# Optimization experiments

Measured on AMD Instinct MI355X. Metric: run time of the kernel, lower is better.

## Reference

```python
import jax, jax.numpy as jnp
import numpy as np

D = 64          # embed_dim
NH = 4          # nhead
DH = D // NH    # head dim
FF = 2048       # TransformerEncoderLayer default dim_feedforward
V = 1_000_000   # vocab (num items)
MAX_LEN = 50
INSERT_LEN = 10
EPS = 1e-5
N_LAYERS = 2


def setup_inputs() -> dict:
    key = jax.random.key(0)
    ks = jax.random.split(key, 8)
    s = 0.02
    return {
        "ht": jax.random.normal(ks[0], (D,), dtype=jnp.float32),
        "item_emb": jax.random.normal(ks[1], (V, D), dtype=jnp.float32) * s,
        "pos_emb": jax.random.normal(ks[2], (MAX_LEN, D), dtype=jnp.float32) * s,
        "in_proj_w": jax.random.normal(ks[3], (N_LAYERS, 3 * D, D), dtype=jnp.float32) * s,
        "in_proj_b": jnp.zeros((N_LAYERS, 3 * D), jnp.float32),
        "out_w": jax.random.normal(ks[4], (N_LAYERS, D, D), dtype=jnp.float32) * s,
        "out_b": jnp.zeros((N_LAYERS, D), jnp.float32),
        "ln1_w": jnp.ones((N_LAYERS, D), jnp.float32),
        "ln1_b": jnp.zeros((N_LAYERS, D), jnp.float32),
        "ln2_w": jnp.ones((N_LAYERS, D), jnp.float32),
        "ln2_b": jnp.zeros((N_LAYERS, D), jnp.float32),
        "ffn1_w": jax.random.normal(ks[5], (N_LAYERS, FF, D), dtype=jnp.float32) * s,
        "ffn1_b": jnp.zeros((N_LAYERS, FF), jnp.float32),
        "ffn2_w": jax.random.normal(ks[6], (N_LAYERS, D, FF), dtype=jnp.float32) * s,
        "ffn2_b": jnp.zeros((N_LAYERS, D), jnp.float32),
    }


def _ln(x, w, b):
    m = jnp.mean(x, axis=-1, keepdims=True)
    v = jnp.mean(jnp.square(x - m), axis=-1, keepdims=True)
    return (x - m) * jax.lax.rsqrt(v + EPS) * w + b


def _encoder_layer(x, ipw, ipb, ow, ob, l1w, l1b, l2w, l2b, f1w, f1b, f2w, f2b):
    # x: [S, D]; post-norm TransformerEncoderLayer (PyTorch defaults, eval mode)
    S = x.shape[0]
    qkv = x @ ipw.T + ipb                      # [S, 3D]
    q, k, v = jnp.split(qkv, 3, axis=-1)
    q = q.reshape(S, NH, DH)
    k = k.reshape(S, NH, DH)
    v = v.reshape(S, NH, DH)
    scores = jnp.einsum('shd,thd->hst', q, k) / jnp.sqrt(jnp.float32(DH))
    attn = jax.nn.softmax(scores, axis=-1)
    o = jnp.einsum('hst,thd->shd', attn, v).reshape(S, D)
    o = o @ ow.T + ob
    x = _ln(x + o, l1w, l1b)
    ff = jax.nn.relu(x @ f1w.T + f1b) @ f2w.T + f2b
    return _ln(x + ff, l2w, l2b)


def reference(ht, item_emb, pos_emb, in_proj_w, in_proj_b, out_w, out_b,
              ln1_w, ln1_b, ln2_w, ln2_b, ffn1_w, ffn1_b, ffn2_w, ffn2_b):
    gen = []         # generated item indices (traced int scalars)
    logits_all = []
    for _ in range(INSERT_LEN):
        if gen:
            gen_embed = item_emb[jnp.stack(gen)]             # [t, D]
            stack = jnp.concatenate([ht[None, :], gen_embed], axis=0)
        else:
            stack = ht[None, :]
        S = stack.shape[0]
        x = stack + pos_emb[:S]
        for l in range(N_LAYERS):
            x = _encoder_layer(x, in_proj_w[l], in_proj_b[l], out_w[l], out_b[l],
                               ln1_w[l], ln1_b[l], ln2_w[l], ln2_b[l],
                               ffn1_w[l], ffn1_b[l], ffn2_w[l], ffn2_b[l])
        logits = x[-1] @ item_emb.T                           # [V]
        gen.append(jnp.argmax(logits))
        logits_all.append(logits)
    return jnp.stack(logits_all), jnp.stack(gen)
```

## Files before the change

### kernel.cpp

```cpp
#include <hip/hip_runtime.h>

typedef unsigned long long u64;
typedef unsigned int u32;
typedef unsigned short u16;

#define V_ 1000000
#define STEPS_ 10
#define EPS_ 1e-5f
#define MARGIN_ 0.02f

__device__ __forceinline__ u64 pack_best(float v, int idx) {
    u32 u = __float_as_uint(v);
    u = (u & 0x80000000u) ? ~u : (u | 0x80000000u);
    return ((u64)u << 32) | (u64)(~(u32)idx);
}
__device__ __forceinline__ int unpack_idx(u64 p) { return (int)(~(u32)p); }
__device__ __forceinline__ float unpack_val(u64 p) {
    u32 hi = (u32)(p >> 32);
    return __uint_as_float((hi & 0x80000000u) ? (hi ^ 0x80000000u) : ~hi);
}
__device__ __forceinline__ u64 shfl_xor_u64(u64 v, int m) {
    u32 lo = (u32)v, hi = (u32)(v >> 32);
    lo = (u32)__shfl_xor((int)lo, m);
    hi = (u32)__shfl_xor((int)hi, m);
    return ((u64)hi << 32) | lo;
}
__device__ __forceinline__ u16 f2bf(float f) {
    u32 u = __float_as_uint(f);
    u += 0x7fffu + ((u >> 16) & 1u);
    return (u16)(u >> 16);
}
__device__ __forceinline__ float bf_lo(u32 u) { return __uint_as_float(u << 16); }
__device__ __forceinline__ float bf_hi(u32 u) { return __uint_as_float(u & 0xffff0000u); }

__device__ int resolve_argmax(const u64* __restrict__ cand,
                              const float* __restrict__ item_emb,
                              const float* __restrict__ y_last,
                              const float* __restrict__ lnw,
                              const float* __restrict__ lnb,
                              float* s_xl, int* s_list, u64* s_wm,
                              int* s_cnt, u64* s_best)
{
    const int tid = threadIdx.x;
    if (tid < 64) {
        float v = y_last[tid];
        float m = v;
        #pragma unroll
        for (int o = 1; o < 64; o <<= 1) m += __shfl_xor(m, o);
        m *= (1.f / 64.f);
        float df = v - m;
        float var = df * df;
        #pragma unroll
        for (int o = 1; o < 64; o <<= 1) var += __shfl_xor(var, o);
        var *= (1.f / 64.f);
        s_xl[tid] = df * (1.f / sqrtf(var + EPS_)) * lnw[tid] + lnb[tid];
    }
    if (tid == 0) { *s_cnt = 0; *s_best = 0ull; }
    __syncthreads();

    u64 m = 0ull;
    for (int i = tid; i < 2048; i += 256) { u64 c = cand[i]; if (c > m) m = c; }
    #pragma unroll
    for (int o = 1; o < 64; o <<= 1) { u64 x = shfl_xor_u64(m, o); if (x > m) m = x; }
    if ((tid & 63) == 0) s_wm[tid >> 6] = m;
    __syncthreads();
    if (tid == 0) {
        u64 b = s_wm[0];
        for (int i = 1; i < 4; i++) if (s_wm[i] > b) b = s_wm[i];
        s_wm[0] = b;
    }
    __syncthreads();

    float thr = unpack_val(s_wm[0]) - MARGIN_;
    for (int i = tid; i < 2048; i += 256) {
        if (unpack_val(cand[i]) >= thr) {
            int p = atomicAdd(s_cnt, 1);
            if (p < 64) s_list[p] = unpack_idx(cand[i]);
        }
    }
    __syncthreads();
    int n = *s_cnt; if (n > 64) n = 64;
    const int wid = tid >> 6, lane = tid & 63;
    for (int c = wid; c < n; c += 4) {
        int row = s_list[c];
        float p = s_xl[lane] * item_emb[(size_t)row * 64 + lane];
        #pragma unroll
        for (int o = 1; o < 64; o <<= 1) p += __shfl_xor(p, o);
        if (lane == 0) atomicMax(s_best, pack_best(p, row));
    }
    __syncthreads();
    return unpack_idx(*s_best);
}

__global__ __launch_bounds__(256) void attn0_kernel(
    const float* __restrict__ ht, const float* __restrict__ item_emb,
    const float* __restrict__ pos_emb,
    const float* __restrict__ ipw, const float* __restrict__ ipb,
    const float* __restrict__ ow,  const float* __restrict__ ob,
    const float* __restrict__ l1w, const float* __restrict__ l1b,
    const float* __restrict__ l2w1, const float* __restrict__ l2b1,
    const u64* __restrict__ cand, const float* __restrict__ y_last,
    int* __restrict__ gen_idx, float* __restrict__ gen_out,
    const float* __restrict__ f1w, const float* __restrict__ f1b,
    float* __restrict__ xp0, float* __restrict__ hbuf, int t)
{
    const int S = t + 1;
    const int tid = threadIdx.x;
    __shared__ float x[640], qkv[1920], att[400], o_[640], y2[640], xps[640];
    __shared__ float rm[10], rr[10], xl[64];
    __shared__ int list[64], cnt;
    __shared__ u64 wm[4], best;

    int newidx = -1;
    if (t > 0) {
        newidx = resolve_argmax(cand, item_emb, y_last, l2w1, l2b1,
                                xl, list, wm, &cnt, &best);
        if (blockIdx.x == 0 && tid == 0) {
            gen_idx[t - 1] = newidx;
            gen_out[t - 1] = (float)newidx;
        }
    }
    __syncthreads();

    for (int i = tid; i < S * 64; i += 256) {
        int s = i >> 6, d = i & 63;
        float base;
        if (s == 0) base = ht[d];
        else {
            int gi = (s == t) ? newidx : gen_idx[s - 1];
            base = item_emb[(size_t)gi * 64 + d];
        }
        x[i] = base + pos_emb[i];
    }
    __syncthreads();

    for (int i = tid; i < S * 192; i += 256) {
        int s = i / 192, j = i % 192;
        float acc = ipb[j];
        const float4* wr = (const float4*)(ipw + j * 64);
        const float4* xr = (const float4*)(x + s * 64);
        #pragma unroll
        for (int k = 0; k < 16; k++) {
            float4 w4 = wr[k], xv = xr[k];
            acc += w4.x * xv.x + w4.y * xv.y + w4.z * xv.z + w4.w * xv.w;
        }
        qkv[i] = acc;
    }
    __syncthreads();

    for (int i = tid; i < 4 * S * S; i += 256) {
        int h = i / (S * S), r = i % (S * S);
        int si = r / S, ti = r % S;
        const float* qr = qkv + si * 192 + h * 16;
        const float* kr = qkv + ti * 192 + 64 + h * 16;
        float acc = 0.f;
        #pragma unroll
        for (int k = 0; k < 16; k++) acc += qr[k] * kr[k];
        att[(h * S + si) * S + ti] = acc * 0.25f;
    }
    __syncthreads();

    for (int i = tid; i < 4 * S; i += 256) {
        float* row = att + i * S;
        float mx = row[0];
        for (int j = 1; j < S; j++) mx = fmaxf(mx, row[j]);
        float sm = 0.f;
        for (int j = 0; j < S; j++) { float e = expf(row[j] - mx); row[j] = e; sm += e; }
        float inv = 1.f / sm;
        for (int j = 0; j < S; j++) row[j] *= inv;
    }
    __syncthreads();

    for (int i = tid; i < S * 64; i += 256) {
        int si = i >> 6, d = i & 63, h = d >> 4, dh = d & 15;
        const float* ar = att + (h * S + si) * S;
        float acc = 0.f;
        for (int ti = 0; ti < S; ti++) acc += ar[ti] * qkv[ti * 192 + 128 + h * 16 + dh];
        o_[i] = acc;
    }
    __syncthreads();

    for (int i = tid; i < S * 64; i += 256) {
        int s = i >> 6, d = i & 63;
        float acc = ob[d] + x[i];
        const float4* wr = (const float4*)(ow + d * 64);
        const float4* orow = (const float4*)(o_ + s * 64);
        #pragma unroll
        for (int k = 0; k < 16; k++) {
            float4 w4 = wr[k], ov = orow[k];
            acc += w4.x * ov.x + w4.y * ov.y + w4.z * ov.z + w4.w * ov.w;
        }
        y2[i] = acc;
    }
    __syncthreads();

    if (tid < S) {
        const float* yr = y2 + tid * 64;
        float m = 0.f;
        for (int k = 0; k < 64; k++) m += yr[k];
        m *= (1.f / 64.f);
        float v = 0.f;
        for (int k = 0; k < 64; k++) { float df = yr[k] - m; v += df * df; }
        rm[tid] = m;
        rr[tid] = 1.f / sqrtf(v * (1.f / 64.f) + EPS_);
    }
    __syncthreads();
    for (int i = tid; i < S * 64; i += 256) {
        int s = i >> 6, d = i & 63;
        float v = (y2[i] - rm[s]) * rr[s] * l1w[d] + l1b[d];
        xps[i] = v;
        xp0[i] = v;
    }
    __syncthreads();

    const int jl = tid >> 4, kp = tid & 15;
    const int j = blockIdx.x * 16 + jl;
    float4 w4 = ((const float4*)(f1w + (size_t)j * 64))[kp];
    float b1 = f1b[j];
    for (int s = 0; s < S; s++) {
        float4 xv = ((const float4*)(xps + s * 64))[kp];
        float p = w4.x * xv.x + w4.y * xv.y + w4.z * xv.z + w4.w * xv.w;
        p += __shfl_xor(p, 1);
        p += __shfl_xor(p, 2);
        p += __shfl_xor(p, 4);
        p += __shfl_xor(p, 8);
        if (kp == 0) hbuf[s * 2048 + j] = fmaxf(p + b1, 0.f);
    }
}

__global__ __launch_bounds__(256) void ffn2_full_kernel(
    const float* __restrict__ f2w0, const float* __restrict__ f2b0,
    const float* __restrict__ hbuf, const float* __restrict__ xp0,
    float* __restrict__ y0, int S)
{
    const int tid = threadIdx.x, d = blockIdx.x;
    const float4* w4 = (const float4*)(f2w0 + (size_t)d * 2048 + tid * 8);
    float4 w0 = w4[0], w1 = w4[1];
    __shared__ float sw[4][10];
    for (int s = 0; s < S; s++) {
        const float4* h4 = (const float4*)(hbuf + s * 2048 + tid * 8);
        float4 h0 = h4[0], h1 = h4[1];
        float p = w0.x * h0.x + w0.y * h0.y + w0.z * h0.z + w0.w * h0.w
                + w1.x * h1.x + w1.y * h1.y + w1.z * h1.z + w1.w * h1.w;
        #pragma unroll
        for (int o = 1; o < 64; o <<= 1) p += __shfl_xor(p, o);
        if ((tid & 63) == 0) sw[tid >> 6][s] = p;
    }
    __syncthreads();
    if (tid < S)
        y0[tid * 64 + d] = sw[0][tid] + sw[1][tid] + sw[2][tid] + sw[3][tid]
                         + f2b0[d] + xp0[tid * 64 + d];
}

__global__ __launch_bounds__(256) void attn1_kernel(
    const float* __restrict__ y0,
    const float* __restrict__ l2w0, const float* __restrict__ l2b0,
    const float* __restrict__ ipw1, const float* __restrict__ ipb1,
    const float* __restrict__ ow1,  const float* __restrict__ ob1,
    const float* __restrict__ l1w1, const float* __restrict__ l1b1,
    const float* __restrict__ f1w1, const float* __restrict__ f1b1,
    float* __restrict__ xp1_last, float* __restrict__ hbuf, int S)
{
    const int tid = threadIdx.x;
    __shared__ float y0s[640], x1[640], qkv[1920], att[40], ol[64], y2l[64], xpl[64];
    __shared__ float rm[10], rr[10];

    for (int i = tid; i < S * 64; i += 256) y0s[i] = y0[i];
    __syncthreads();
    if (tid < S) {
        const float* yr = y0s + tid * 64;
        float m = 0.f;
        for (int k = 0; k < 64; k++) m += yr[k];
        m *= (1.f / 64.f);
        float v = 0.f;
        for (int k = 0; k < 64; k++) { float df = yr[k] - m; v += df * df; }
        rm[tid] = m;
        rr[tid] = 1.f / sqrtf(v * (1.f / 64.f) + EPS_);
    }
    __syncthreads();
    for (int i = tid; i < S * 64; i += 256) {
        int s = i >> 6, d = i & 63;
        x1[i] = (y0s[i] - rm[s]) * rr[s] * l2w0[d] + l2b0[d];
    }
    __syncthreads();

    for (int i = tid; i < S * 192; i += 256) {
        int s = i / 192, j = i % 192;
        float acc = ipb1[j];
        const float4* wr = (const float4*)(ipw1 + j * 64);
        const float4* xr = (const float4*)(x1 + s * 64);
        #pragma unroll
        for (int k = 0; k < 16; k++) {
            float4 w4 = wr[k], xv = xr[k];
            acc += w4.x * xv.x + w4.y * xv.y + w4.z * xv.z + w4.w * xv.w;
        }
        qkv[i] = acc;
    }
    __syncthreads();

    for (int i = tid; i < 4 * S; i += 256) {
        int h = i / S, ti = i % S;
        const float* qr = qkv + (S - 1) * 192 + h * 16;
        const float* kr = qkv + ti * 192 + 64 + h * 16;
        float acc = 0.f;
        #pragma unroll
        for (int k = 0; k < 16; k++) acc += qr[k] * kr[k];
        att[h * S + ti] = acc * 0.25f;
    }
    __syncthreads();
    if (tid < 4) {
        float* row = att + tid * S;
        float mx = row[0];
        for (int j = 1; j < S; j++) mx = fmaxf(mx, row[j]);
        float sm = 0.f;
        for (int j = 0; j < S; j++) { float e = expf(row[j] - mx); row[j] = e; sm += e; }
        float inv = 1.f / sm;
        for (int j = 0; j < S; j++) row[j] *= inv;
    }
    __syncthreads();
    if (tid < 64) {
        int h = tid >> 4, dh = tid & 15;
        const float* ar = att + h * S;
        float acc = 0.f;
        for (int ti = 0; ti < S; ti++) acc += ar[ti] * qkv[ti * 192 + 128 + h * 16 + dh];
        ol[tid] = acc;
    }
    __syncthreads();
    if (tid < 64) {
        float acc = ob1[tid] + x1[(S - 1) * 64 + tid];
        const float* wr = ow1 + tid * 64;
        for (int k = 0; k < 64; k++) acc += ol[k] * wr[k];
        y2l[tid] = acc;
    }
    __syncthreads();
    if (tid < 64) {
        float v = y2l[tid];
        float m = v;
        #pragma unroll
        for (int o = 1; o < 64; o <<= 1) m += __shfl_xor(m, o);
        m *= (1.f / 64.f);
        float df = v - m;
        float var = df * df;
        #pragma unroll
        for (int o = 1; o < 64; o <<= 1) var += __shfl_xor(var, o);
        float r = 1.f / sqrtf(var * (1.f / 64.f) + EPS_);
        float xv = df * r * l1w1[tid] + l1b1[tid];
        xpl[tid] = xv;
        xp1_last[tid] = xv;
    }
    __syncthreads();

    const int jl = tid >> 4, kp = tid & 15;
    const int j = blockIdx.x * 16 + jl;
    float4 w4 = ((const float4*)(f1w1 + (size_t)j * 64))[kp];
    float4 xv = ((const float4*)xpl)[kp];
    float p = w4.x * xv.x + w4.y * xv.y + w4.z * xv.z + w4.w * xv.w;
    p += __shfl_xor(p, 1);
    p += __shfl_xor(p, 2);
    p += __shfl_xor(p, 4);
    p += __shfl_xor(p, 8);
    if (kp == 0) hbuf[j] = fmaxf(p + f1b1[j], 0.f);
}

__global__ __launch_bounds__(256) void ffn2_last_kernel(
    const float* __restrict__ f2w1, const float* __restrict__ f2b1,
    const float* __restrict__ hbuf, const float* __restrict__ xp1_last,
    float* __restrict__ y_last)
{
    const int tid = threadIdx.x, d = blockIdx.x;
    const float4* w4 = (const float4*)(f2w1 + (size_t)d * 2048 + tid * 8);
    const float4* h4 = (const float4*)(hbuf + tid * 8);
    float4 w0 = w4[0], w1 = w4[1], h0 = h4[0], h1 = h4[1];
    float p = w0.x * h0.x + w0.y * h0.y + w0.z * h0.z + w0.w * h0.w
            + w1.x * h1.x + w1.y * h1.y + w1.z * h1.z + w1.w * h1.w;
    #pragma unroll
    for (int o = 1; o < 64; o <<= 1) p += __shfl_xor(p, o);
    __shared__ float sw[4];
    if ((tid & 63) == 0) sw[tid >> 6] = p;
    __syncthreads();
    if (tid == 0) y_last[d] = sw[0] + sw[1] + sw[2] + sw[3] + f2b1[d] + xp1_last[d];
}

__global__ __launch_bounds__(256) void logits_f32_kernel(
    const float* __restrict__ item_emb, const float* __restrict__ y_last,
    const float* __restrict__ lnw, const float* __restrict__ lnb,
    float* __restrict__ out, u64* __restrict__ cand, u16* __restrict__ emb16)
{
    const int tid = threadIdx.x;
    __shared__ float xl[64];
    if (tid < 64) {
        float v = y_last[tid];
        float m = v;
        #pragma unroll
        for (int o = 1; o < 64; o <<= 1) m += __shfl_xor(m, o);
        m *= (1.f / 64.f);
        float df = v - m;
        float var = df * df;
        #pragma unroll
        for (int o = 1; o < 64; o <<= 1) var += __shfl_xor(var, o);
        float r = 1.f / sqrtf(var * (1.f / 64.f) + EPS_);
        xl[tid] = df * r * lnw[tid] + lnb[tid];
    }
    __syncthreads();

    const int l16 = tid & 15;
    float4 q = ((const float4*)xl)[l16];
    const int group0 = (blockIdx.x * 256 + tid) >> 4;
    const int ngroups = (gridDim.x * 256) >> 4;
    u64 lb = 0ull;

    for (int row = group0; row < V_; row += ngroups) {
        float4 e = ((const float4*)(item_emb + (size_t)row * 64))[l16];
        ushort4 us;
        us.x = f2bf(e.x); us.y = f2bf(e.y); us.z = f2bf(e.z); us.w = f2bf(e.w);
        *(ushort4*)(emb16 + (size_t)row * 64 + l16 * 4) = us;
        float p = q.x * e.x + q.y * e.y + q.z * e.z + q.w * e.w;
        p += __shfl_xor(p, 1);
        p += __shfl_xor(p, 2);
        p += __shfl_xor(p, 4);
        p += __shfl_xor(p, 8);
        if (l16 == 0) {
            out[row] = p;
            u64 pk = pack_best(p, row);
            if (pk > lb) lb = pk;
        }
    }
    #pragma unroll
    for (int o = 1; o < 64; o <<= 1) { u64 x = shfl_xor_u64(lb, o); if (x > lb) lb = x; }
    __shared__ u64 sb[4];
    if ((tid & 63) == 0) sb[tid >> 6] = lb;
    __syncthreads();
    if (tid == 0) {
        u64 b = sb[0];
        for (int i = 1; i < 4; i++) if (sb[i] > b) b = sb[i];
        cand[blockIdx.x] = b;
    }
}

__global__ __launch_bounds__(256) void logits_bf16_kernel(
    const u16* __restrict__ emb16, const float* __restrict__ y_last,
    const float* __restrict__ lnw, const float* __restrict__ lnb,
    float* __restrict__ out, u64* __restrict__ cand)
{
    const int tid = threadIdx.x;
    __shared__ float xl[64];
    if (tid < 64) {
        float v = y_last[tid];
        float m = v;
        #pragma unroll
        for (int o = 1; o < 64; o <<= 1) m += __shfl_xor(m, o);
        m *= (1.f / 64.f);
        float df = v - m;
        float var = df * df;
        #pragma unroll
        for (int o = 1; o < 64; o <<= 1) var += __shfl_xor(var, o);
        float r = 1.f / sqrtf(var * (1.f / 64.f) + EPS_);
        xl[tid] = df * r * lnw[tid] + lnb[tid];
    }
    __syncthreads();

    const int j8 = tid & 7;
    float q[8];
    #pragma unroll
    for (int i = 0; i < 8; i++) q[i] = xl[j8 * 8 + i];
    const int group0 = (blockIdx.x * 256 + tid) >> 3;
    const int ngroups = (gridDim.x * 256) >> 3;
    const uint4* base = (const uint4*)emb16;
    u64 lb = 0ull;

    for (int row = group0; row < V_; row += ngroups) {
        uint4 u = base[(size_t)row * 8 + j8];
        float p = q[0] * bf_lo(u.x) + q[1] * bf_hi(u.x)
                + q[2] * bf_lo(u.y) + q[3] * bf_hi(u.y)
                + q[4] * bf_lo(u.z) + q[5] * bf_hi(u.z)
                + q[6] * bf_lo(u.w) + q[7] * bf_hi(u.w);
        p += __shfl_xor(p, 1);
        p += __shfl_xor(p, 2);
        p += __shfl_xor(p, 4);
        if (j8 == 0) {
            out[row] = p;
            u64 pk = pack_best(p, row);
            if (pk > lb) lb = pk;
        }
    }
    #pragma unroll
    for (int o = 1; o < 64; o <<= 1) { u64 x = shfl_xor_u64(lb, o); if (x > lb) lb = x; }
    __shared__ u64 sb[4];
    if ((tid & 63) == 0) sb[tid >> 6] = lb;
    __syncthreads();
    if (tid == 0) {
        u64 b = sb[0];
        for (int i = 1; i < 4; i++) if (sb[i] > b) b = sb[i];
        cand[blockIdx.x] = b;
    }
}

__global__ __launch_bounds__(256) void finalize_kernel(
    const u64* __restrict__ cand, const float* __restrict__ item_emb,
    const float* __restrict__ y_last,
    const float* __restrict__ lnw, const float* __restrict__ lnb,
    float* __restrict__ gen_out)
{
    __shared__ float xl[64];
    __shared__ int list[64], cnt;
    __shared__ u64 wm[4], best;
    int r = resolve_argmax(cand, item_emb, y_last, lnw, lnb, xl, list, wm, &cnt, &best);
    if (threadIdx.x == 0) gen_out[STEPS_ - 1] = (float)r;
}

extern "C" void kernel_launch(void* const* d_in, const int* in_sizes, int n_in,
                              void* d_out, int out_size, void* d_ws, size_t ws_size,
                              hipStream_t stream) {
    const float* ht       = (const float*)d_in[0];
    const float* item_emb = (const float*)d_in[1];
    const float* pos_emb  = (const float*)d_in[2];
    const float* ipw      = (const float*)d_in[3];
    const float* ipb      = (const float*)d_in[4];
    const float* ow       = (const float*)d_in[5];
    const float* ob       = (const float*)d_in[6];
    const float* l1w      = (const float*)d_in[7];
    const float* l1b      = (const float*)d_in[8];
    const float* l2w      = (const float*)d_in[9];
    const float* l2b      = (const float*)d_in[10];
    const float* f1w      = (const float*)d_in[11];
    const float* f1b      = (const float*)d_in[12];
    const float* f2w      = (const float*)d_in[13];
    const float* f2b      = (const float*)d_in[14];

    float* out = (float*)d_out;
    char* ws = (char*)d_ws;
    int*   gen_idx = (int*)ws;
    float* xp0     = (float*)(ws + 64);
    float* xp1l    = (float*)(ws + 2624);
    float* y_last  = (float*)(ws + 2880);
    float* y0      = (float*)(ws + 3136);
    float* hbuf    = (float*)(ws + 8192);
    u64*   cand    = (u64*)(ws + 90112);
    u16*   emb16   = (u16*)(ws + 131072);
    float* gen_out = out + (size_t)STEPS_ * V_;

    for (int t = 0; t < STEPS_; t++) {
        const int S = t + 1;
        attn0_kernel<<<128, 256, 0, stream>>>(
            ht, item_emb, pos_emb, ipw, ipb, ow, ob, l1w, l1b,
            l2w + 64, l2b + 64, cand, y_last, gen_idx, gen_out,
            f1w, f1b, xp0, hbuf, t);
        ffn2_full_kernel<<<64, 256, 0, stream>>>(f2w, f2b, hbuf, xp0, y0, S);
        attn1_kernel<<<128, 256, 0, stream>>>(
            y0, l2w, l2b, ipw + 192 * 64, ipb + 192, ow + 64 * 64, ob + 64,
            l1w + 64, l1b + 64, f1w + 2048 * 64, f1b + 2048, xp1l, hbuf, S);
        ffn2_last_kernel<<<64, 256, 0, stream>>>(
            f2w + (size_t)64 * 2048, f2b + 64, hbuf, xp1l, y_last);
        if (t == 0)
            logits_f32_kernel<<<2048, 256, 0, stream>>>(
                item_emb, y_last, l2w + 64, l2b + 64, out, cand, emb16);
        else
            logits_bf16_kernel<<<2048, 256, 0, stream>>>(
                emb16, y_last, l2w + 64, l2b + 64, out + (size_t)t * V_, cand);
    }
    finalize_kernel<<<1, 256, 0, stream>>>(
        cand, item_emb, y_last, l2w + 64, l2b + 64, gen_out);
}
```

Before: 1.029 ms.

## Fuse four per-step encoder kernels into one persistent kernel with grid barriers

Replaces the attn0, ffn2_full, attn1 and ffn2_last launches per decode step with a single 128-block encoder kernel. The kernel uses atomic-counter grid barriers between the FFN1, FFN2 and layer-1 phases, and the counter is reset once by an init kernel. The goal is to cut kernel launch and inter-kernel gaps, about 30 fewer launches in total. In exchange it relies on all 128 blocks being co-resident for the spin barrier, and every block now redundantly recomputes layer-1 attention after reading y0 from global memory.

```diff
diff --git a/kernel.cpp b/kernel.cpp
--- a/kernel.cpp
+++ b/kernel.cpp
@@ -8,6 +8,7 @@
 #define STEPS_ 10
 #define EPS_ 1e-5f
 #define MARGIN_ 0.02f
+#define NBLK_ 128
 
 __device__ __forceinline__ u64 pack_best(float v, int idx) {
     u32 u = __float_as_uint(v);
@@ -32,6 +33,18 @@
 }
 __device__ __forceinline__ float bf_lo(u32 u) { return __uint_as_float(u << 16); }
 __device__ __forceinline__ float bf_hi(u32 u) { return __uint_as_float(u & 0xffff0000u); }
+
+__device__ __forceinline__ void grid_barrier(u32* cnt, u32 target) {
+    __syncthreads();
+    if (threadIdx.x == 0) {
+        __threadfence();
+        __hip_atomic_fetch_add(cnt, 1u, __ATOMIC_ACQ_REL, __HIP_MEMORY_SCOPE_AGENT);
+        while (__hip_atomic_load(cnt, __ATOMIC_ACQUIRE, __HIP_MEMORY_SCOPE_AGENT) < target) {
+            __builtin_amdgcn_s_sleep(2);
+        }
+    }
+    __syncthreads();
+}
 
 __device__ int resolve_argmax(const u64* __restrict__ cand,
                               const float* __restrict__ item_emb,
@@ -92,20 +105,27 @@
     return unpack_idx(*s_best);
 }
 
-__global__ __launch_bounds__(256) void attn0_kernel(
+__global__ void init_kernel(u32* bar) { if (threadIdx.x == 0) *bar = 0u; }
+
+__global__ __launch_bounds__(256) void encoder_kernel(
     const float* __restrict__ ht, const float* __restrict__ item_emb,
     const float* __restrict__ pos_emb,
     const float* __restrict__ ipw, const float* __restrict__ ipb,
     const float* __restrict__ ow,  const float* __restrict__ ob,
     const float* __restrict__ l1w, const float* __restrict__ l1b,
-    const float* __restrict__ l2w1, const float* __restrict__ l2b1,
-    const u64* __restrict__ cand, const float* __restrict__ y_last,
-    int* __restrict__ gen_idx, float* __restrict__ gen_out,
+    const float* __restrict__ l2w, const float* __restrict__ l2b,
     const float* __restrict__ f1w, const float* __restrict__ f1b,
-    float* __restrict__ xp0, float* __restrict__ hbuf, int t)
+    const float* __restrict__ f2w, const float* __restrict__ f2b,
+    const u64* __restrict__ cand, int* __restrict__ gen_idx,
+    float* __restrict__ gen_out, float* __restrict__ y0,
+    float* __restrict__ y_last, float* __restrict__ hbuf,
+    u32* __restrict__ bar, int t)
 {
     const int S = t + 1;
     const int tid = threadIdx.x;
+    const int bid = blockIdx.x;
+    const u32 base = (u32)(3 * t) * NBLK_;
+
     __shared__ float x[640], qkv[1920], att[400], o_[640], y2[640], xps[640];
     __shared__ float rm[10], rr[10], xl[64];
     __shared__ int list[64], cnt;
@@ -113,9 +133,9 @@
 
     int newidx = -1;
     if (t > 0) {
-        newidx = resolve_argmax(cand, item_emb, y_last, l2w1, l2b1,
+        newidx = resolve_argmax(cand, item_emb, y_last, l2w + 64, l2b + 64,
                                 xl, list, wm, &cnt, &best);
-        if (blockIdx.x == 0 && tid == 0) {
+        if (bid == 0 && tid == 0) {
             gen_idx[t - 1] = newidx;
             gen_out[t - 1] = (float)newidx;
         }
@@ -124,13 +144,13 @@
 
     for (int i = tid; i < S * 64; i += 256) {
         int s = i >> 6, d = i & 63;
-        float base;
-        if (s == 0) base = ht[d];
+        float basev;
+        if (s == 0) basev = ht[d];
         else {
             int gi = (s == t) ? newidx : gen_idx[s - 1];
-            base = item_emb[(size_t)gi * 64 + d];
-        }
-        x[i] = base + pos_emb[i];
+            basev = item_emb[(size_t)gi * 64 + d];
+        }
+        x[i] = basev + pos_emb[i];
     }
     __syncthreads();
 
@@ -207,68 +227,56 @@
     __syncthreads();
     for (int i = tid; i < S * 64; i += 256) {
         int s = i >> 6, d = i & 63;
-        float v = (y2[i] - rm[s]) * rr[s] * l1w[d] + l1b[d];
-        xps[i] = v;
-        xp0[i] = v;
-    }
-    __syncthreads();
-
-    const int jl = tid >> 4, kp = tid & 15;
-    const int j = blockIdx.x * 16 + jl;
-    float4 w4 = ((const float4*)(f1w + (size_t)j * 64))[kp];
-    float b1 = f1b[j];
-    for (int s = 0; s < S; s++) {
-        float4 xv = ((const float4*)(xps + s * 64))[kp];
-        float p = w4.x * xv.x + w4.y * xv.y + w4.z * xv.z + w4.w * xv.w;
-        p += __shfl_xor(p, 1);
-        p += __shfl_xor(p, 2);
-        p += __shfl_xor(p, 4);
-        p += __shfl_xor(p, 8);
-        if (kp == 0) hbuf[s * 2048 + j] = fmaxf(p + b1, 0.f);
-    }
-}
-
-__global__ __launch_bounds__(256) void ffn2_full_kernel(
-    const float* __restrict__ f2w0, const float* __restrict__ f2b0,
-    const float* __restrict__ hbuf, const float* __restrict__ xp0,
-    float* __restrict__ y0, int S)
-{
-    const int tid = threadIdx.x, d = blockIdx.x;
-    const float4* w4 = (const float4*)(f2w0 + (size_t)d * 2048 + tid * 8);
-    float4 w0 = w4[0], w1 = w4[1];
-    __shared__ float sw[4][10];
-    for (int s = 0; s < S; s++) {
-        const float4* h4 = (const float4*)(hbuf + s * 2048 + tid * 8);
-        float4 h0 = h4[0], h1 = h4[1];
-        float p = w0.x * h0.x + w0.y * h0.y + w0.z * h0.z + w0.w * h0.w
-                + w1.x * h1.x + w1.y * h1.y + w1.z * h1.z + w1.w * h1.w;
-        #pragma unroll
-        for (int o = 1; o < 64; o <<= 1) p += __shfl_xor(p, o);
-        if ((tid & 63) == 0) sw[tid >> 6][s] = p;
-    }
-    __syncthreads();
-    if (tid < S)
-        y0[tid * 64 + d] = sw[0][tid] + sw[1][tid] + sw[2][tid] + sw[3][tid]
-                         + f2b0[d] + xp0[tid * 64 + d];
-}
-
-__global__ __launch_bounds__(256) void attn1_kernel(
-    const float* __restrict__ y0,
-    const float* __restrict__ l2w0, const float* __restrict__ l2b0,
-    const float* __restrict__ ipw1, const float* __restrict__ ipb1,
-    const float* __restrict__ ow1,  const float* __restrict__ ob1,
-    const float* __restrict__ l1w1, const float* __restrict__ l1b1,
-    const float* __restrict__ f1w1, const float* __restrict__ f1b1,
-    float* __restrict__ xp1_last, float* __restrict__ hbuf, int S)
-{
-    const int tid = threadIdx.x;
-    __shared__ float y0s[640], x1[640], qkv[1920], att[40], ol[64], y2l[64], xpl[64];
-    __shared__ float rm[10], rr[10];
-
-    for (int i = tid; i < S * 64; i += 256) y0s[i] = y0[i];
+        xps[i] = (y2[i] - rm[s]) * rr[s] * l1w[d] + l1b[d];
+    }
+    __syncthreads();
+
+    {
+        const int jl = tid >> 4, kp = tid & 15;
+        const int j = bid * 16 + jl;
+        float4 w4 = ((const float4*)(f1w + (size_t)j * 64))[kp];
+        float b1 = f1b[j];
+        for (int s = 0; s < S; s++) {
+            float4 xv = ((const float4*)(xps + s * 64))[kp];
+            float p = w4.x * xv.x + w4.y * xv.y + w4.z * xv.z + w4.w * xv.w;
+            p += __shfl_xor(p, 1);
+            p += __shfl_xor(p, 2);
+            p += __shfl_xor(p, 4);
+            p += __shfl_xor(p, 8);
+            if (kp == 0) hbuf[s * 2048 + j] = fmaxf(p + b1, 0.f);
+        }
+    }
+    grid_barrier(bar, base + NBLK_);
+
+    {
+        const int d = bid & 63, half = bid >> 6;
+        const int sh = (S + 1) >> 1;
+        const int s0 = half * sh, s1 = (half ? S : sh);
+        const float4* w4p = (const float4*)(f2w + (size_t)d * 2048 + tid * 8);
+        float4 w0 = w4p[0], w1 = w4p[1];
+        for (int s = s0; s < s1; s++) {
+            const float4* h4 = (const float4*)(hbuf + s * 2048 + tid * 8);
+            float4 h0 = h4[0], h1 = h4[1];
+            float p = w0.x * h0.x + w0.y * h0.y + w0.z * h0.z + w0.w * h0.w
+                    + w1.x * h1.x + w1.y * h1.y + w1.z * h1.z + w1.w * h1.w;
+            #pragma unroll
+            for (int o = 1; o < 64; o <<= 1) p += __shfl_xor(p, o);
+            if ((tid & 63) == 0) wm[tid >> 6] = __float_as_uint(p);
+            __syncthreads();
+            if (tid == 0) {
+                float v = __uint_as_float((u32)wm[0]) + __uint_as_float((u32)wm[1])
+                        + __uint_as_float((u32)wm[2]) + __uint_as_float((u32)wm[3]);
+                y0[s * 64 + d] = v + f2b[d] + xps[s * 64 + d];
+            }
+            __syncthreads();
+        }
+    }
+    grid_barrier(bar, base + 2 * NBLK_);
+
+    for (int i = tid; i < S * 64; i += 256) y2[i] = y0[i];
     __syncthreads();
     if (tid < S) {
-        const float* yr = y0s + tid * 64;
+        const float* yr = y2 + tid * 64;
         float m = 0.f;
         for (int k = 0; k < 64; k++) m += yr[k];
         m *= (1.f / 64.f);
@@ -280,15 +288,16 @@
     __syncthreads();
     for (int i = tid; i < S * 64; i += 256) {
         int s = i >> 6, d = i & 63;
-        x1[i] = (y0s[i] - rm[s]) * rr[s] * l2w0[d] + l2b0[d];
-    }
-    __syncthreads();
-
+        x[i] = (y2[i] - rm[s]) * rr[s] * l2w[d] + l2b[d];
+    }
+    __syncthreads();
+
+    const float* ipw1 = ipw + 192 * 64;
     for (int i = tid; i < S * 192; i += 256) {
         int s = i / 192, j = i % 192;
-        float acc = ipb1[j];
+        float acc = ipb[192 + j];
         const float4* wr = (const float4*)(ipw1 + j * 64);
-        const float4* xr = (const float4*)(x1 + s * 64);
+        const float4* xr = (const float4*)(x + s * 64);
         #pragma unroll
         for (int k = 0; k < 16; k++) {
             float4 w4 = wr[k], xv = xr[k];
@@ -323,18 +332,18 @@
         const float* ar = att + h * S;
         float acc = 0.f;
         for (int ti = 0; ti < S; ti++) acc += ar[ti] * qkv[ti * 192 + 128 + h * 16 + dh];
-        ol[tid] = acc;
+        o_[tid] = acc;
     }
     __syncthreads();
     if (tid < 64) {
-        float acc = ob1[tid] + x1[(S - 1) * 64 + tid];
-        const float* wr = ow1 + tid * 64;
-        for (int k = 0; k < 64; k++) acc += ol[k] * wr[k];
-        y2l[tid] = acc;
+        float acc = ob[64 + tid] + x[(S - 1) * 64 + tid];
+        const float* wr = ow + 64 * 64 + tid * 64;
+        for (int k = 0; k < 64; k++) acc += o_[k] * wr[k];
+        y2[tid] = acc;
     }
     __syncthreads();
     if (tid < 64) {
-        float v = y2l[tid];
+        float v = y2[tid];
         float m = v;
         #pragma unroll
         for (int o = 1; o < 64; o <<= 1) m += __shfl_xor(m, o);
@@ -344,41 +353,38 @@
         #pragma unroll
         for (int o = 1; o < 64; o <<= 1) var += __shfl_xor(var, o);
         float r = 1.f / sqrtf(var * (1.f / 64.f) + EPS_);
-        float xv = df * r * l1w1[tid] + l1b1[tid];
-        xpl[tid] = xv;
-        xp1_last[tid] = xv;
-    }
-    __syncthreads();
-
-    const int jl = tid >> 4, kp = tid & 15;
-    const int j = blockIdx.x * 16 + jl;
-    float4 w4 = ((const float4*)(f1w1 + (size_t)j * 64))[kp];
-    float4 xv = ((const float4*)xpl)[kp];
-    float p = w4.x * xv.x + w4.y * xv.y + w4.z * xv.z + w4.w * xv.w;
-    p += __shfl_xor(p, 1);
-    p += __shfl_xor(p, 2);
-    p += __shfl_xor(p, 4);
-    p += __shfl_xor(p, 8);
-    if (kp == 0) hbuf[j] = fmaxf(p + f1b1[j], 0.f);
-}
-
-__global__ __launch_bounds__(256) void ffn2_last_kernel(
-    const float* __restrict__ f2w1, const float* __restrict__ f2b1,
-    const float* __restrict__ hbuf, const float* __restrict__ xp1_last,
-    float* __restrict__ y_last)
-{
-    const int tid = threadIdx.x, d = blockIdx.x;
-    const float4* w4 = (const float4*)(f2w1 + (size_t)d * 2048 + tid * 8);
-    const float4* h4 = (const float4*)(hbuf + tid * 8);
-    float4 w0 = w4[0], w1 = w4[1], h0 = h4[0], h1 = h4[1];
-    float p = w0.x * h0.x + w0.y * h0.y + w0.z * h0.z + w0.w * h0.w
-            + w1.x * h1.x + w1.y * h1.y + w1.z * h1.z + w1.w * h1.w;
-    #pragma unroll
-    for (int o = 1; o < 64; o <<= 1) p += __shfl_xor(p, o);
-    __shared__ float sw[4];
-    if ((tid & 63) == 0) sw[tid >> 6] = p;
-    __syncthreads();
-    if (tid == 0) y_last[d] = sw[0] + sw[1] + sw[2] + sw[3] + f2b1[d] + xp1_last[d];
+        xps[tid] = df * r * l1w[64 + tid] + l1b[64 + tid];
+    }
+    __syncthreads();
+
+    {
+        const int jl = tid >> 4, kp = tid & 15;
+        const int j = bid * 16 + jl;
+        float4 w4 = ((const float4*)(f1w + (size_t)(2048 + j) * 64))[kp];
+        float4 xv = ((const float4*)xps)[kp];
+        float p = w4.x * xv.x + w4.y * xv.y + w4.z * xv.z + w4.w * xv.w;
+        p += __shfl_xor(p, 1);
+        p += __shfl_xor(p, 2);
+        p += __shfl_xor(p, 4);
+        p += __shfl_xor(p, 8);
+        if (kp == 0) hbuf[j] = fmaxf(p + f1b[2048 + j], 0.f);
+    }
+    grid_barrier(bar, base + 3 * NBLK_);
+
+    if (bid < 64) {
+        const int d = bid;
+        const float4* w4p = (const float4*)(f2w + (size_t)(64 + d) * 2048 + tid * 8);
+        const float4* h4 = (const float4*)(hbuf + tid * 8);
+        float4 w0 = w4p[0], w1 = w4p[1], h0 = h4[0], h1 = h4[1];
+        float p = w0.x * h0.x + w0.y * h0.y + w0.z * h0.z + w0.w * h0.w
+                + w1.x * h1.x + w1.y * h1.y + w1.z * h1.z + w1.w * h1.w;
+        #pragma unroll
+        for (int o = 1; o < 64; o <<= 1) p += __shfl_xor(p, o);
+        __shared__ float sw[4];
+        if ((tid & 63) == 0) sw[tid >> 6] = p;
+        __syncthreads();
+        if (tid == 0) y_last[d] = sw[0] + sw[1] + sw[2] + sw[3] + f2b[64 + d] + xps[d];
+    }
 }
 
 __global__ __launch_bounds__(256) void logits_f32_kernel(
@@ -530,27 +536,19 @@
     float* out = (float*)d_out;
     char* ws = (char*)d_ws;
     int*   gen_idx = (int*)ws;
-    float* xp0     = (float*)(ws + 64);
-    float* xp1l    = (float*)(ws + 2624);
-    float* y_last  = (float*)(ws + 2880);
-    float* y0      = (float*)(ws + 3136);
-    float* hbuf    = (float*)(ws + 8192);
+    u32*   bar     = (u32*)(ws + 128);
+    float* y_last  = (float*)(ws + 256);
+    float* y0      = (float*)(ws + 512);
+    float* hbuf    = (float*)(ws + 4096);
     u64*   cand    = (u64*)(ws + 90112);
     u16*   emb16   = (u16*)(ws + 131072);
     float* gen_out = out + (size_t)STEPS_ * V_;
 
+    init_kernel<<<1, 64, 0, stream>>>(bar);
     for (int t = 0; t < STEPS_; t++) {
-        const int S = t + 1;
-        attn0_kernel<<<128, 256, 0, stream>>>(
-            ht, item_emb, pos_emb, ipw, ipb, ow, ob, l1w, l1b,
-            l2w + 64, l2b + 64, cand, y_last, gen_idx, gen_out,
-            f1w, f1b, xp0, hbuf, t);
-        ffn2_full_kernel<<<64, 256, 0, stream>>>(f2w, f2b, hbuf, xp0, y0, S);
-        attn1_kernel<<<128, 256, 0, stream>>>(
-            y0, l2w, l2b, ipw + 192 * 64, ipb + 192, ow + 64 * 64, ob + 64,
-            l1w + 64, l1b + 64, f1w + 2048 * 64, f1b + 2048, xp1l, hbuf, S);
-        ffn2_last_kernel<<<64, 256, 0, stream>>>(
-            f2w + (size_t)64 * 2048, f2b + 64, hbuf, xp1l, y_last);
+        encoder_kernel<<<NBLK_, 256, 0, stream>>>(
+            ht, item_emb, pos_emb, ipw, ipb, ow, ob, l1w, l1b, l2w, l2b,
+            f1w, f1b, f2w, f2b, cand, gen_idx, gen_out, y0, y_last, hbuf, bar, t);
         if (t == 0)
             logits_f32_kernel<<<2048, 256, 0, stream>>>(
                 item_emb, y_last, l2w + 64, l2b + 64, out, cand, emb16);
```

Result: slower. 1.161 ms (+12.8%).
